# Performance work log

Measured on AMD Instinct MI355X. Metric: run time of the kernel, lower is better.

The kernel has to match this reference:

```python
import jax, jax.numpy as jnp
import numpy as np


def setup_inputs() -> dict:
    key = jax.random.key(0)
    ks = jax.random.split(key, 9)
    B, T, D, U = 512, 1024, 64, 128
    inp = {
        'inputs': jax.random.normal(ks[0], (B, T, D), dtype=jnp.float32),
        'W_f': jax.random.normal(ks[1], (D, U), dtype=jnp.float32) * 0.05,
        'U_f': jax.random.normal(ks[2], (U, U), dtype=jnp.float32) * 0.05,
        'b_f': jnp.zeros((U,), dtype=jnp.float32),
        'W_i': jax.random.normal(ks[3], (D, U), dtype=jnp.float32) * 0.05,
        'U_i': jax.random.normal(ks[4], (U, U), dtype=jnp.float32) * 0.05,
        'b_i': jnp.zeros((U,), dtype=jnp.float32),
        'W_c': jax.random.normal(ks[5], (D, U), dtype=jnp.float32) * 0.05,
        'U_c': jax.random.normal(ks[6], (U, U), dtype=jnp.float32) * 0.05,
        'b_c': jnp.zeros((U,), dtype=jnp.float32),
        'W_o': jax.random.normal(ks[7], (D, U), dtype=jnp.float32) * 0.05,
        'U_o': jax.random.normal(ks[8], (U, U), dtype=jnp.float32) * 0.05,
        'b_o': jnp.zeros((U,), dtype=jnp.float32),
    }
    return inp


def _lstm(inputs, W_f, U_f, b_f, W_i, U_i, b_i, W_c, U_c, b_c, W_o, U_o, b_o):
    B, T, D = inputs.shape
    U = W_f.shape[1]
    # Precompute all input-to-gate projections in one batched GEMM per gate: [B,T,U]
    xf = jnp.einsum('btd,du->btu', inputs, W_f) + b_f
    xi = jnp.einsum('btd,du->btu', inputs, W_i) + b_i
    xc = jnp.einsum('btd,du->btu', inputs, W_c) + b_c
    xo = jnp.einsum('btd,du->btu', inputs, W_o) + b_o
    # time-major stacked gate inputs: [T, B, 4, U]
    xg = jnp.stack([xf, xi, xc, xo], axis=2).transpose(1, 0, 2, 3)
    # concatenated recurrent weights: [U, 4U]
    U_all = jnp.concatenate([U_f, U_i, U_c, U_o], axis=1)

    def step(carry, x_t):
        h, c = carry
        # x_t: [B, 4, U]
        rec = (h @ U_all).reshape(B, 4, U)
        g = x_t + rec
        f = jax.nn.sigmoid(g[:, 0])
        i = jax.nn.sigmoid(g[:, 1])
        c_tilde = jnp.tanh(g[:, 2])
        o = jax.nn.sigmoid(g[:, 3])
        c_new = f * c + i * c_tilde
        h_new = o * jnp.tanh(c_new)
        return (h_new, c_new), None

    h0 = jnp.zeros((B, U), dtype=inputs.dtype)
    c0 = jnp.zeros((B, U), dtype=inputs.dtype)
    (h, c), _ = jax.lax.scan(step, (h0, c0), xg)
    return h


def reference(inputs, W_f, U_f, b_f, W_i, U_i, b_i, W_c, U_c, b_c, W_o, U_o, b_o):
    return _lstm(inputs, W_f, U_f, b_f, W_i, U_i, b_i, W_c, U_c, b_c, W_o, U_o, b_o)
```

## Files before the change

### kernel.cpp

```cpp
#include <hip/hip_runtime.h>
#include <stdint.h>


typedef __attribute__((ext_vector_type(8))) short short8;
typedef __attribute__((ext_vector_type(4))) float floatx4;
typedef __attribute__((ext_vector_type(4))) int   intx4;
typedef __attribute__((ext_vector_type(8))) int   intx8;

#define B_SZ   512
#define T_SZ   1024
#define D_SZ   64
#define U_SZ   128
#define ROWS   2
#define NBLK   (B_SZ / ROWS)
#define NTHR   512
#define A1STRB 160
#define GXSTR  524
#define L2E    1.4426950408889634f

__device__ __forceinline__ short f2bf(float f) {
    uint32_t u = __builtin_bit_cast(uint32_t, f);
    uint32_t r = (u + 0x7fffu + ((u >> 16) & 1u)) >> 16;
    return (short)r;
}
__device__ __forceinline__ int cvt2bf(float lo, float hi) {
    int r;
    asm("v_cvt_pk_bf16_f32 %0, %1, %2" : "=v"(r) : "v"(lo), "v"(hi));
    return r;
}
__device__ __forceinline__ short8 pk8(float4 a, float4 b) {
    intx4 t = {cvt2bf(a.x, a.y), cvt2bf(a.z, a.w), cvt2bf(b.x, b.y), cvt2bf(b.z, b.w)};
    return __builtin_bit_cast(short8, t);
}
__device__ __forceinline__ float fsig2(float e) {
    return __builtin_amdgcn_rcpf(1.0f + __builtin_amdgcn_exp2f(e));
}
__device__ __forceinline__ float fth2(float e) {
    return 1.0f - 2.0f * __builtin_amdgcn_rcpf(1.0f + __builtin_amdgcn_exp2f(e));
}
__device__ __forceinline__ float ftanh(float x) {
    return 1.0f - 2.0f * __builtin_amdgcn_rcpf(1.0f + __builtin_amdgcn_exp2f(2.0f * L2E * x));
}
__device__ __forceinline__ void sync_lds() {
    asm volatile("s_waitcnt lgkmcnt(0)\n\ts_barrier" ::: "memory");
}

__global__ __launch_bounds__(NTHR, 2) void lstm_persistent(
    const float* __restrict__ xin,
    const float* __restrict__ Wf, const float* __restrict__ Uf, const float* __restrict__ bfp,
    const float* __restrict__ Wi, const float* __restrict__ Ui, const float* __restrict__ bip,
    const float* __restrict__ Wc, const float* __restrict__ Uc, const float* __restrict__ bcp,
    const float* __restrict__ Wo, const float* __restrict__ Uo, const float* __restrict__ bop,
    float* __restrict__ out)
{
    __shared__ float Gx[2][16 * GXSTR];
    __shared__ __align__(8) char A1[2][2 * A1STRB];

    const int tid  = threadIdx.x;
    const int wave = tid >> 6;
    const int lane = tid & 63;
    const int quad = lane >> 4;
    const int nlo  = lane & 15;
    const int blk  = blockIdx.x;

    const float* Wg[4] = {Wf, Wi, Wc, Wo};
    const float* Ug[4] = {Uf, Ui, Uc, Uo};
    const float* Bg[4] = {bfp, bip, bcp, bop};
    const float scg[4] = {-L2E, -L2E, 2.0f * L2E, -L2E};

    const int  u_s  = 16 * wave + nlo;
    const int  prow = quad >> 1;
    const bool wr   = (quad & 1) == 0;

    intx8 bU8[4];
#pragma unroll
    for (int gt = 0; gt < 4; ++gt)
#pragma unroll
        for (int d = 0; d < 8; ++d) {
            const int k0 = quad * 32 + d * 4;
            int pk = __builtin_amdgcn_cvt_pk_fp8_f32(
                Ug[gt][(k0 + 0) * U_SZ + u_s], Ug[gt][(k0 + 1) * U_SZ + u_s], 0, 0);
            pk = __builtin_amdgcn_cvt_pk_fp8_f32(
                Ug[gt][(k0 + 2) * U_SZ + u_s], Ug[gt][(k0 + 3) * U_SZ + u_s], pk, 1);
            bU8[gt][d] = pk;
        }

    short8 bWp[4][2];
    float  bw[4];
#pragma unroll
    for (int gt = 0; gt < 4; ++gt) {
        bw[gt] = Bg[gt][u_s];
#pragma unroll
        for (int kt = 0; kt < 2; ++kt)
#pragma unroll
            for (int jj = 0; jj < 8; ++jj) {
                int k = kt * 32 + quad * 8 + jj;
                bWp[gt][kt][jj] = f2bf(Wg[gt][k * U_SZ + u_s]);
            }
    }

    for (int i = tid; i < 2 * 2 * A1STRB; i += NTHR) ((char*)A1)[i] = 0;

    const int brow  = nlo & 1;
    const int t_off = nlo >> 1;
    const float* xg = xin + ((size_t)(blk * ROWS + brow) * T_SZ) * D_SZ + quad * 8;

    float4 p0 = *(const float4*)(xg + (size_t)t_off * D_SZ + 0);
    float4 p1 = *(const float4*)(xg + (size_t)t_off * D_SZ + 4);
    float4 p2 = *(const float4*)(xg + (size_t)t_off * D_SZ + 32);
    float4 p3 = *(const float4*)(xg + (size_t)t_off * D_SZ + 36);
    float4 q0 = *(const float4*)(xg + (size_t)(8 + t_off) * D_SZ + 0);
    float4 q1 = *(const float4*)(xg + (size_t)(8 + t_off) * D_SZ + 4);
    float4 q2 = *(const float4*)(xg + (size_t)(8 + t_off) * D_SZ + 32);
    float4 q3 = *(const float4*)(xg + (size_t)(8 + t_off) * D_SZ + 36);

    short8 xa0 = pk8(p0, p1);
    short8 xa1 = pk8(p2, p3);
#pragma unroll
    for (int gt = 0; gt < 4; ++gt) {
        floatx4 acc = (floatx4){0.f, 0.f, 0.f, 0.f};
        acc = __builtin_amdgcn_mfma_f32_16x16x32_bf16(xa0, bWp[gt][0], acc, 0, 0, 0);
        acc = __builtin_amdgcn_mfma_f32_16x16x32_bf16(xa1, bWp[gt][1], acc, 0, 0, 0);
#pragma unroll
        for (int r = 0; r < 4; ++r)
            Gx[0][(quad * 4 + r) * GXSTR + 4 * u_s + gt] = (acc[r] + bw[gt]) * scg[gt];
    }
    xa0 = pk8(q0, q1);
    xa1 = pk8(q2, q3);
    float4 xq0 = *(const float4*)(xg + (size_t)(16 + t_off) * D_SZ + 0);
    float4 xq1 = *(const float4*)(xg + (size_t)(16 + t_off) * D_SZ + 4);
    float4 xq2 = *(const float4*)(xg + (size_t)(16 + t_off) * D_SZ + 32);
    float4 xq3 = *(const float4*)(xg + (size_t)(16 + t_off) * D_SZ + 36);
    __syncthreads();

    float  c_st = 0.0f;
    short8 xn0 = xa0, xn1 = xa1;
    for (int g = 0; g < 128; ++g) {
        const float* GxR = &Gx[g & 1][0];
        float*       GxW = &Gx[(g + 1) & 1][0];
#pragma unroll
        for (int j = 0; j < 8; ++j) {
            __builtin_amdgcn_s_setprio(1);
            const char* ap = &A1[j & 1][(nlo >> 3) * A1STRB + quad * 32];
            intx4 alo = *(const intx4*)(ap);
            intx4 ahi = *(const intx4*)(ap + 16);
            floatx4 gx = *(const floatx4*)&GxR[(2 * j + prow) * GXSTR + 4 * u_s];
            intx8 a8 = {alo.x, alo.y, alo.z, alo.w, ahi.x, ahi.y, ahi.z, ahi.w};

            floatx4 acc[4];
#pragma unroll
            for (int gt = 0; gt < 4; ++gt) {
                floatx4 z = (floatx4){0.f, 0.f, 0.f, 0.f};
                acc[gt] = __builtin_amdgcn_mfma_scale_f32_16x16x128_f8f6f4(
                    a8, bU8[gt], z, 0, 0, 0, 0x7f7f7f7f, 0, 0x7f7f7f7f);
            }

            float fg = fsig2(__builtin_fmaf(acc[0][0], -L2E, gx[0]));
            float ig = fsig2(__builtin_fmaf(acc[1][0], -L2E, gx[1]));
            float ct = fth2 (__builtin_fmaf(acc[2][0], 2.0f * L2E, gx[2]));
            float og = fsig2(__builtin_fmaf(acc[3][0], -L2E, gx[3]));
            float c  = fg * c_st + ig * ct;
            float h  = og * ftanh(c);
            c_st = c;

            if (g == 127 && j == 7) {
                if (wr) out[(size_t)(blk * ROWS + prow) * U_SZ + u_s] = h;
            } else if (wr) {
                int pk = __builtin_amdgcn_cvt_pk_fp8_f32(h, h, 0, 0);
                A1[(j & 1) ^ 1][prow * A1STRB + u_s] = (char)(pk & 0xff);
            }
            __builtin_amdgcn_s_setprio(0);

            if (j == 0 && g <= 125) {
                xn0 = pk8(xq0, xq1);
                xn1 = pk8(xq2, xq3);
            }
            if (j == 2 && g <= 124) {
                const float* b = xg + (size_t)(8 * (g + 3) + t_off) * D_SZ;
                xq0 = *(const float4*)(b + 0);
                xq1 = *(const float4*)(b + 4);
                xq2 = *(const float4*)(b + 32);
                xq3 = *(const float4*)(b + 36);
            }
            if ((j & 1) && g < 127) {
                const int gt = j >> 1;
                floatx4 acc2 = (floatx4){0.f, 0.f, 0.f, 0.f};
                acc2 = __builtin_amdgcn_mfma_f32_16x16x32_bf16(xa0, bWp[gt][0], acc2, 0, 0, 0);
                acc2 = __builtin_amdgcn_mfma_f32_16x16x32_bf16(xa1, bWp[gt][1], acc2, 0, 0, 0);
#pragma unroll
                for (int r = 0; r < 4; ++r)
                    GxW[(quad * 4 + r) * GXSTR + 4 * u_s + gt] = (acc2[r] + bw[gt]) * scg[gt];
            }
            sync_lds();
        }
        xa0 = xn0; xa1 = xn1;
    }
}

extern "C" void kernel_launch(void* const* d_in, const int* in_sizes, int n_in,
                              void* d_out, int out_size, void* d_ws, size_t ws_size,
                              hipStream_t stream) {
    (void)in_sizes; (void)n_in; (void)d_ws; (void)ws_size; (void)out_size;
    const float* xin = (const float*)d_in[0];
    const float* Wf  = (const float*)d_in[1];
    const float* Uf  = (const float*)d_in[2];
    const float* bf  = (const float*)d_in[3];
    const float* Wi  = (const float*)d_in[4];
    const float* Ui  = (const float*)d_in[5];
    const float* bi  = (const float*)d_in[6];
    const float* Wc  = (const float*)d_in[7];
    const float* Uc  = (const float*)d_in[8];
    const float* bc  = (const float*)d_in[9];
    const float* Wo  = (const float*)d_in[10];
    const float* Uo  = (const float*)d_in[11];
    const float* bo  = (const float*)d_in[12];
    float* out = (float*)d_out;

    hipLaunchKernelGGL(lstm_persistent, dim3(NBLK), dim3(NTHR), 0, stream,
                       xin, Wf, Uf, bf, Wi, Ui, bi, Wc, Uc, bc, Wo, Uo, bo, out);
}
```

Before: 577.0 us.

## Specialize warps: split recurrent and input-projection work into separate wave groups

Doubles the block to 1024 threads. Waves 0-7 run only the recurrent fp8 MFMA, gate math and h writes, at raised priority. Waves 8-15 run only the input projection GEMM and prefetch x into the double-buffered Gx. The aim is to take the x loads and the projection off the serial critical path of the recurrence, so both overlap. The costs are larger blocks, a barrier across 16 waves at every step, and __syncthreads placed inside divergent branches, which may be fragile.

```diff
diff --git a/kernel.cpp b/kernel.cpp
--- a/kernel.cpp
+++ b/kernel.cpp
@@ -13,7 +13,7 @@
 #define U_SZ   128
 #define ROWS   2
 #define NBLK   (B_SZ / ROWS)
-#define NTHR   512
+#define NTHR   1024
 #define A1STRB 160
 #define GXSTR  524
 #define L2E    1.4426950408889634f
@@ -45,7 +45,7 @@
     asm volatile("s_waitcnt lgkmcnt(0)\n\ts_barrier" ::: "memory");
 }
 
-__global__ __launch_bounds__(NTHR, 2) void lstm_persistent(
+__global__ __launch_bounds__(NTHR, 4) void lstm_persistent(
     const float* __restrict__ xin,
     const float* __restrict__ Wf, const float* __restrict__ Uf, const float* __restrict__ bfp,
     const float* __restrict__ Wi, const float* __restrict__ Ui, const float* __restrict__ bip,
@@ -68,132 +68,143 @@
     const float* Bg[4] = {bfp, bip, bcp, bop};
     const float scg[4] = {-L2E, -L2E, 2.0f * L2E, -L2E};
 
-    const int  u_s  = 16 * wave + nlo;
-    const int  prow = quad >> 1;
-    const bool wr   = (quad & 1) == 0;
-
-    intx8 bU8[4];
-#pragma unroll
-    for (int gt = 0; gt < 4; ++gt)
-#pragma unroll
-        for (int d = 0; d < 8; ++d) {
-            const int k0 = quad * 32 + d * 4;
-            int pk = __builtin_amdgcn_cvt_pk_fp8_f32(
-                Ug[gt][(k0 + 0) * U_SZ + u_s], Ug[gt][(k0 + 1) * U_SZ + u_s], 0, 0);
-            pk = __builtin_amdgcn_cvt_pk_fp8_f32(
-                Ug[gt][(k0 + 2) * U_SZ + u_s], Ug[gt][(k0 + 3) * U_SZ + u_s], pk, 1);
-            bU8[gt][d] = pk;
-        }
-
-    short8 bWp[4][2];
-    float  bw[4];
-#pragma unroll
-    for (int gt = 0; gt < 4; ++gt) {
-        bw[gt] = Bg[gt][u_s];
-#pragma unroll
-        for (int kt = 0; kt < 2; ++kt)
-#pragma unroll
-            for (int jj = 0; jj < 8; ++jj) {
-                int k = kt * 32 + quad * 8 + jj;
-                bWp[gt][kt][jj] = f2bf(Wg[gt][k * U_SZ + u_s]);
+    if (wave < 8) {
+        __builtin_amdgcn_s_setprio(1);
+        const int  prow = quad >> 1;
+        const bool wr   = (quad & 1) == 0;
+        const int  u_s  = 16 * wave + nlo;
+
+        intx8 bU8[4];
+#pragma unroll
+        for (int gt = 0; gt < 4; ++gt)
+#pragma unroll
+            for (int d = 0; d < 8; ++d) {
+                const int k0 = quad * 32 + d * 4;
+                int pk = __builtin_amdgcn_cvt_pk_fp8_f32(
+                    Ug[gt][(k0 + 0) * U_SZ + u_s], Ug[gt][(k0 + 1) * U_SZ + u_s], 0, 0);
+                pk = __builtin_amdgcn_cvt_pk_fp8_f32(
+                    Ug[gt][(k0 + 2) * U_SZ + u_s], Ug[gt][(k0 + 3) * U_SZ + u_s], pk, 1);
+                bU8[gt][d] = pk;
             }
-    }
-
-    for (int i = tid; i < 2 * 2 * A1STRB; i += NTHR) ((char*)A1)[i] = 0;
-
-    const int brow  = nlo & 1;
-    const int t_off = nlo >> 1;
-    const float* xg = xin + ((size_t)(blk * ROWS + brow) * T_SZ) * D_SZ + quad * 8;
-
-    float4 p0 = *(const float4*)(xg + (size_t)t_off * D_SZ + 0);
-    float4 p1 = *(const float4*)(xg + (size_t)t_off * D_SZ + 4);
-    float4 p2 = *(const float4*)(xg + (size_t)t_off * D_SZ + 32);
-    float4 p3 = *(const float4*)(xg + (size_t)t_off * D_SZ + 36);
-    float4 q0 = *(const float4*)(xg + (size_t)(8 + t_off) * D_SZ + 0);
-    float4 q1 = *(const float4*)(xg + (size_t)(8 + t_off) * D_SZ + 4);
-    float4 q2 = *(const float4*)(xg + (size_t)(8 + t_off) * D_SZ + 32);
-    float4 q3 = *(const float4*)(xg + (size_t)(8 + t_off) * D_SZ + 36);
-
-    short8 xa0 = pk8(p0, p1);
-    short8 xa1 = pk8(p2, p3);
-#pragma unroll
-    for (int gt = 0; gt < 4; ++gt) {
-        floatx4 acc = (floatx4){0.f, 0.f, 0.f, 0.f};
-        acc = __builtin_amdgcn_mfma_f32_16x16x32_bf16(xa0, bWp[gt][0], acc, 0, 0, 0);
-        acc = __builtin_amdgcn_mfma_f32_16x16x32_bf16(xa1, bWp[gt][1], acc, 0, 0, 0);
-#pragma unroll
-        for (int r = 0; r < 4; ++r)
-            Gx[0][(quad * 4 + r) * GXSTR + 4 * u_s + gt] = (acc[r] + bw[gt]) * scg[gt];
-    }
-    xa0 = pk8(q0, q1);
-    xa1 = pk8(q2, q3);
-    float4 xq0 = *(const float4*)(xg + (size_t)(16 + t_off) * D_SZ + 0);
-    float4 xq1 = *(const float4*)(xg + (size_t)(16 + t_off) * D_SZ + 4);
-    float4 xq2 = *(const float4*)(xg + (size_t)(16 + t_off) * D_SZ + 32);
-    float4 xq3 = *(const float4*)(xg + (size_t)(16 + t_off) * D_SZ + 36);
-    __syncthreads();
-
-    float  c_st = 0.0f;
-    short8 xn0 = xa0, xn1 = xa1;
-    for (int g = 0; g < 128; ++g) {
-        const float* GxR = &Gx[g & 1][0];
-        float*       GxW = &Gx[(g + 1) & 1][0];
-#pragma unroll
-        for (int j = 0; j < 8; ++j) {
-            __builtin_amdgcn_s_setprio(1);
-            const char* ap = &A1[j & 1][(nlo >> 3) * A1STRB + quad * 32];
-            intx4 alo = *(const intx4*)(ap);
-            intx4 ahi = *(const intx4*)(ap + 16);
-            floatx4 gx = *(const floatx4*)&GxR[(2 * j + prow) * GXSTR + 4 * u_s];
-            intx8 a8 = {alo.x, alo.y, alo.z, alo.w, ahi.x, ahi.y, ahi.z, ahi.w};
-
-            floatx4 acc[4];
-#pragma unroll
-            for (int gt = 0; gt < 4; ++gt) {
-                floatx4 z = (floatx4){0.f, 0.f, 0.f, 0.f};
-                acc[gt] = __builtin_amdgcn_mfma_scale_f32_16x16x128_f8f6f4(
-                    a8, bU8[gt], z, 0, 0, 0, 0x7f7f7f7f, 0, 0x7f7f7f7f);
+        float c_st = 0.0f;
+
+        for (int i = tid; i < 2 * 2 * A1STRB; i += 512) ((char*)A1)[i] = 0;
+        __syncthreads();
+
+        for (int g = 0; g < 128; ++g) {
+            const float* GxR = &Gx[g & 1][0];
+#pragma unroll
+            for (int j = 0; j < 8; ++j) {
+                const char* ap = &A1[j & 1][(nlo >> 3) * A1STRB + quad * 32];
+                intx4 alo = *(const intx4*)(ap);
+                intx4 ahi = *(const intx4*)(ap + 16);
+                floatx4 gx = *(const floatx4*)&GxR[(2 * j + prow) * GXSTR + 4 * u_s];
+                intx8 a8 = {alo.x, alo.y, alo.z, alo.w, ahi.x, ahi.y, ahi.z, ahi.w};
+                const floatx4 z = (floatx4){0.f, 0.f, 0.f, 0.f};
+
+                floatx4 acc[4];
+#pragma unroll
+                for (int gt = 0; gt < 4; ++gt)
+                    acc[gt] = __builtin_amdgcn_mfma_scale_f32_16x16x128_f8f6f4(
+                        a8, bU8[gt], z, 0, 0, 0, 0x7f7f7f7f, 0, 0x7f7f7f7f);
+
+                float fg = fsig2(__builtin_fmaf(acc[0][0], -L2E, gx[0]));
+                float ig = fsig2(__builtin_fmaf(acc[1][0], -L2E, gx[1]));
+                float ct = fth2(__builtin_fmaf(acc[2][0], 2.0f * L2E, gx[2]));
+                float og = fsig2(__builtin_fmaf(acc[3][0], -L2E, gx[3]));
+
+                float c = fg * c_st + ig * ct;
+                float h = og * ftanh(c);
+                c_st = c;
+
+                if (g == 127 && j == 7) {
+                    if (wr) out[(size_t)(blk * ROWS + prow) * U_SZ + u_s] = h;
+                } else if (wr) {
+                    int pk = __builtin_amdgcn_cvt_pk_fp8_f32(h, h, 0, 0);
+                    A1[(j & 1) ^ 1][prow * A1STRB + u_s] = (char)(pk & 0xff);
+                }
+                sync_lds();
             }
-
-            float fg = fsig2(__builtin_fmaf(acc[0][0], -L2E, gx[0]));
-            float ig = fsig2(__builtin_fmaf(acc[1][0], -L2E, gx[1]));
-            float ct = fth2 (__builtin_fmaf(acc[2][0], 2.0f * L2E, gx[2]));
-            float og = fsig2(__builtin_fmaf(acc[3][0], -L2E, gx[3]));
-            float c  = fg * c_st + ig * ct;
-            float h  = og * ftanh(c);
-            c_st = c;
-
-            if (g == 127 && j == 7) {
-                if (wr) out[(size_t)(blk * ROWS + prow) * U_SZ + u_s] = h;
-            } else if (wr) {
-                int pk = __builtin_amdgcn_cvt_pk_fp8_f32(h, h, 0, 0);
-                A1[(j & 1) ^ 1][prow * A1STRB + u_s] = (char)(pk & 0xff);
+        }
+    } else {
+        const int p = wave - 8;
+        const int brow  = nlo & 1;
+        const int t_off = nlo >> 1;
+        const int uc    = 16 * p + nlo;
+
+        short8 bWp[4][2];
+        float  bw[4];
+#pragma unroll
+        for (int gt = 0; gt < 4; ++gt) {
+            bw[gt] = Bg[gt][uc];
+#pragma unroll
+            for (int kt = 0; kt < 2; ++kt)
+#pragma unroll
+                for (int jj = 0; jj < 8; ++jj) {
+                    int k = kt * 32 + quad * 8 + jj;
+                    bWp[gt][kt][jj] = f2bf(Wg[gt][k * U_SZ + uc]);
+                }
+        }
+
+        const float* xg = xin + ((size_t)(blk * ROWS + brow) * T_SZ) * D_SZ + quad * 8;
+
+        float4 p0 = *(const float4*)(xg + (size_t)t_off * D_SZ + 0);
+        float4 p1 = *(const float4*)(xg + (size_t)t_off * D_SZ + 4);
+        float4 p2 = *(const float4*)(xg + (size_t)t_off * D_SZ + 32);
+        float4 p3 = *(const float4*)(xg + (size_t)t_off * D_SZ + 36);
+        float4 q0 = *(const float4*)(xg + (size_t)(8 + t_off) * D_SZ + 0);
+        float4 q1 = *(const float4*)(xg + (size_t)(8 + t_off) * D_SZ + 4);
+        float4 q2 = *(const float4*)(xg + (size_t)(8 + t_off) * D_SZ + 32);
+        float4 q3 = *(const float4*)(xg + (size_t)(8 + t_off) * D_SZ + 36);
+
+        short8 xa0 = pk8(p0, p1);
+        short8 xa1 = pk8(p2, p3);
+#pragma unroll
+        for (int gt = 0; gt < 4; ++gt) {
+            floatx4 acc = (floatx4){0.f, 0.f, 0.f, 0.f};
+            acc = __builtin_amdgcn_mfma_f32_16x16x32_bf16(xa0, bWp[gt][0], acc, 0, 0, 0);
+            acc = __builtin_amdgcn_mfma_f32_16x16x32_bf16(xa1, bWp[gt][1], acc, 0, 0, 0);
+#pragma unroll
+            for (int r = 0; r < 4; ++r)
+                Gx[0][(quad * 4 + r) * GXSTR + 4 * uc + gt] = (acc[r] + bw[gt]) * scg[gt];
+        }
+        xa0 = pk8(q0, q1);
+        xa1 = pk8(q2, q3);
+        float4 xq0 = *(const float4*)(xg + (size_t)(16 + t_off) * D_SZ + 0);
+        float4 xq1 = *(const float4*)(xg + (size_t)(16 + t_off) * D_SZ + 4);
+        float4 xq2 = *(const float4*)(xg + (size_t)(16 + t_off) * D_SZ + 32);
+        float4 xq3 = *(const float4*)(xg + (size_t)(16 + t_off) * D_SZ + 36);
+        __syncthreads();
+
+        short8 xn0 = xa0, xn1 = xa1;
+        for (int g = 0; g < 128; ++g) {
+            float* GxW = &Gx[(g + 1) & 1][0];
+#pragma unroll
+            for (int j = 0; j < 8; ++j) {
+                if (j == 0 && g <= 125) {
+                    xn0 = pk8(xq0, xq1);
+                    xn1 = pk8(xq2, xq3);
+                }
+                if (j == 2 && g <= 124) {
+                    const float* b = xg + (size_t)(8 * (g + 3) + t_off) * D_SZ;
+                    xq0 = *(const float4*)(b + 0);
+                    xq1 = *(const float4*)(b + 4);
+                    xq2 = *(const float4*)(b + 32);
+                    xq3 = *(const float4*)(b + 36);
+                }
+                if ((j & 1) && g < 127) {
+                    const int gt = j >> 1;
+                    floatx4 acc = (floatx4){0.f, 0.f, 0.f, 0.f};
+                    acc = __builtin_amdgcn_mfma_f32_16x16x32_bf16(xa0, bWp[gt][0], acc, 0, 0, 0);
+                    acc = __builtin_amdgcn_mfma_f32_16x16x32_bf16(xa1, bWp[gt][1], acc, 0, 0, 0);
+#pragma unroll
+                    for (int r = 0; r < 4; ++r)
+                        GxW[(quad * 4 + r) * GXSTR + 4 * uc + gt] = (acc[r] + bw[gt]) * scg[gt];
+                }
+                sync_lds();
             }
-            __builtin_amdgcn_s_setprio(0);
-
-            if (j == 0 && g <= 125) {
-                xn0 = pk8(xq0, xq1);
-                xn1 = pk8(xq2, xq3);
-            }
-            if (j == 2 && g <= 124) {
-                const float* b = xg + (size_t)(8 * (g + 3) + t_off) * D_SZ;
-                xq0 = *(const float4*)(b + 0);
-                xq1 = *(const float4*)(b + 4);
-                xq2 = *(const float4*)(b + 32);
-                xq3 = *(const float4*)(b + 36);
-            }
-            if ((j & 1) && g < 127) {
-                const int gt = j >> 1;
-                floatx4 acc2 = (floatx4){0.f, 0.f, 0.f, 0.f};
-                acc2 = __builtin_amdgcn_mfma_f32_16x16x32_bf16(xa0, bWp[gt][0], acc2, 0, 0, 0);
-                acc2 = __builtin_amdgcn_mfma_f32_16x16x32_bf16(xa1, bWp[gt][1], acc2, 0, 0, 0);
-#pragma unroll
-                for (int r = 0; r < 4; ++r)
-                    GxW[(quad * 4 + r) * GXSTR + 4 * u_s + gt] = (acc2[r] + bw[gt]) * scg[gt];
-            }
-            sync_lds();
-        }
-        xa0 = xn0; xa1 = xn1;
+            xa0 = xn0; xa1 = xn1;
+        }
     }
 }
 
```

Result: faster. 509.6 us (-11.7%).
